# Kernel optimization log

Measured on AMD Instinct MI355X. Metric: run time of the kernel, lower is better.

## Reference

```python
import jax, jax.numpy as jnp
import numpy as np

NUM_HEADS = 16
EMBED_DIM = 1024
HEAD_DIM = EMBED_DIM // NUM_HEADS


def setup_inputs() -> dict:
    key = jax.random.key(0)
    ks = jax.random.split(key, 9)
    B, S, D = 2, 2048, EMBED_DIM
    s = 1.0 / np.sqrt(D)
    inp = {
        "x": jax.random.normal(ks[0], (B, S, D), dtype=jnp.float32),
        "Wq": jax.random.normal(ks[1], (D, D), dtype=jnp.float32) * s,
        "bq": jnp.zeros((D,), dtype=jnp.float32),
        "Wk": jax.random.normal(ks[2], (D, D), dtype=jnp.float32) * s,
        "bk": jnp.zeros((D,), dtype=jnp.float32),
        "Wv": jax.random.normal(ks[3], (D, D), dtype=jnp.float32) * s,
        "bv": jnp.zeros((D,), dtype=jnp.float32),
        "Wo": jax.random.normal(ks[4], (D, D), dtype=jnp.float32) * s,
        "bo": jnp.zeros((D,), dtype=jnp.float32),
    }
    return inp


def reference(x, Wq, bq, Wk, bk, Wv, bv, Wo, bo):
    B, S, D = x.shape
    H, Hd = NUM_HEADS, HEAD_DIM
    # projections (weights stored [in, out])
    q = (x @ Wq + bq).reshape(B, S, H, Hd).transpose(0, 2, 1, 3)  # [B,H,S,Hd]
    k = (x @ Wk + bk).reshape(B, S, H, Hd).transpose(0, 2, 1, 3)
    v = (x @ Wv + bv).reshape(B, S, H, Hd).transpose(0, 2, 1, 3)
    scores = jnp.einsum("bhqd,bhkd->bhqk", q, k) / jnp.sqrt(jnp.float32(Hd))
    causal = jnp.tril(jnp.ones((S, S), dtype=bool))  # True = keep
    scores = jnp.where(causal, scores, jnp.float32(-jnp.inf))
    attn = jax.nn.softmax(scores, axis=-1)
    ctx = jnp.einsum("bhqk,bhkd->bhqd", attn, v)  # [B,H,S,Hd]
    ctx = ctx.transpose(0, 2, 1, 3).reshape(B, S, D)
    return ctx @ Wo + bo
```

## Files before the change

### kernel.cpp

```cpp
#include <hip/hip_runtime.h>

#define NUMH 16
#define HD   64
#define SEQ  2048
#define NB   2
#define DIM  1024
#define MROWS (NB * SEQ)

typedef __attribute__((ext_vector_type(8))) short short8;
typedef __attribute__((ext_vector_type(4))) float f32x4;
typedef unsigned short u16;
typedef unsigned int u32;

__device__ inline u16 bf16_rn(float f) {
    unsigned u = __float_as_uint(f);
    return (u16)((u + 0x7FFFu + ((u >> 16) & 1u)) >> 16);
}
__device__ inline float bf16f(u16 h) {
    return __uint_as_float(((unsigned)h) << 16);
}

#define GLD16(gp, lp)                                                        \
    __builtin_amdgcn_global_load_lds(                                        \
        (const __attribute__((address_space(1))) void*)(gp),                 \
        (__attribute__((address_space(3))) void*)(lp), 16, 0, 0)

__global__ void convert_split(const float* __restrict__ in,
                              u16* __restrict__ hi, u16* __restrict__ lo, int n4)
{
    for (int i = blockIdx.x * blockDim.x + threadIdx.x; i < n4;
         i += gridDim.x * blockDim.x) {
        const float4 v = ((const float4*)in)[i];
        ushort4 h, l;
        h.x = bf16_rn(v.x); l.x = bf16_rn(v.x - bf16f(h.x));
        h.y = bf16_rn(v.y); l.y = bf16_rn(v.y - bf16f(h.y));
        h.z = bf16_rn(v.z); l.z = bf16_rn(v.z - bf16f(h.z));
        h.w = bf16_rn(v.w); l.w = bf16_rn(v.w - bf16f(h.w));
        ((ushort4*)hi)[i] = h;
        ((ushort4*)lo)[i] = l;
    }
}

__global__ __launch_bounds__(256)
void transpose_split(const float* __restrict__ W,
                     u16* __restrict__ th, u16* __restrict__ tl, float scale)
{
    __shared__ float Ls[32][33];
    const int tx = threadIdx.x & 31, ty = threadIdx.x >> 5;
    const int k0 = blockIdx.x * 32, n0 = blockIdx.y * 32;
#pragma unroll
    for (int i = 0; i < 4; ++i)
        Ls[ty + 8 * i][tx] = W[(size_t)(k0 + ty + 8 * i) * DIM + n0 + tx];
    __syncthreads();
#pragma unroll
    for (int i = 0; i < 4; ++i) {
        const float f = Ls[tx][ty + 8 * i] * scale;
        const u16 h = bf16_rn(f);
        const u16 l = bf16_rn(f - bf16f(h));
        th[(size_t)(n0 + ty + 8 * i) * DIM + k0 + tx] = h;
        tl[(size_t)(n0 + ty + 8 * i) * DIM + k0 + tx] = l;
    }
}

template<int EPI>
__global__ __launch_bounds__(256, 4)
void gemm_split(const u16* __restrict__ Ah, const u16* __restrict__ Al,
                const u16* __restrict__ Bh, const u16* __restrict__ Bl,
                const float* __restrict__ bias, float bscale,
                float* __restrict__ outF, u16* __restrict__ outH,
                u16* __restrict__ outL)
{
    __shared__ u16 AsH[128][32];
    __shared__ u16 AsL[128][32];
    __shared__ u16 BsH[64][32];
    __shared__ u16 BsL[64][32];

    const int tid  = threadIdx.x;
    const int m0   = blockIdx.x * 128;
    const int n0   = blockIdx.y * 64;
    const int wid  = tid >> 6;
    const int lane = tid & 63;
    const int wr   = wid >> 1;
    const int wc   = wid & 1;
    const int fr   = lane & 15;
    const int fg   = lane >> 4;
    const int K    = DIM;

    f32x4 acc[4][2];
#pragma unroll
    for (int i = 0; i < 4; ++i)
#pragma unroll
        for (int j = 0; j < 2; ++j) { f32x4 z = {0.f, 0.f, 0.f, 0.f}; acc[i][j] = z; }

    const int gr = (wid << 4) + (lane >> 2);
    const int gc = (lane & 3) * 8;

    for (int kt = 0; kt < K; kt += 32) {
        __syncthreads();
        GLD16(&Ah[(size_t)(m0 + gr) * K + kt + gc],      &AsH[(wid << 4)][0]);
        GLD16(&Ah[(size_t)(m0 + 64 + gr) * K + kt + gc], &AsH[64 + (wid << 4)][0]);
        GLD16(&Al[(size_t)(m0 + gr) * K + kt + gc],      &AsL[(wid << 4)][0]);
        GLD16(&Al[(size_t)(m0 + 64 + gr) * K + kt + gc], &AsL[64 + (wid << 4)][0]);
        GLD16(&Bh[(size_t)(n0 + gr) * K + kt + gc],      &BsH[(wid << 4)][0]);
        GLD16(&Bl[(size_t)(n0 + gr) * K + kt + gc],      &BsL[(wid << 4)][0]);
        __syncthreads();

        short8 afh[4], afl[4], bfh[2], bfl[2];
#pragma unroll
        for (int i = 0; i < 4; ++i) {
            afh[i] = *(const short8*)&AsH[wr * 64 + i * 16 + fr][fg * 8];
            afl[i] = *(const short8*)&AsL[wr * 64 + i * 16 + fr][fg * 8];
        }
#pragma unroll
        for (int j = 0; j < 2; ++j) {
            bfh[j] = *(const short8*)&BsH[wc * 32 + j * 16 + fr][fg * 8];
            bfl[j] = *(const short8*)&BsL[wc * 32 + j * 16 + fr][fg * 8];
        }
#pragma unroll
        for (int i = 0; i < 4; ++i)
#pragma unroll
            for (int j = 0; j < 2; ++j) {
                acc[i][j] = __builtin_amdgcn_mfma_f32_16x16x32_bf16(afl[i], bfh[j], acc[i][j], 0, 0, 0);
                acc[i][j] = __builtin_amdgcn_mfma_f32_16x16x32_bf16(afh[i], bfl[j], acc[i][j], 0, 0, 0);
                acc[i][j] = __builtin_amdgcn_mfma_f32_16x16x32_bf16(afh[i], bfh[j], acc[i][j], 0, 0, 0);
            }
    }

#pragma unroll
    for (int i = 0; i < 4; ++i)
#pragma unroll
        for (int j = 0; j < 2; ++j) {
            const int col = n0 + wc * 32 + j * 16 + fr;
            const float bv = bias[col] * bscale;
            if (EPI == 2) {
                const int row = m0 + wr * 64 + i * 16 + fg * 4;
                const int b  = row >> 11;
                const int s  = row & (SEQ - 1);
                const int hh = col >> 6;
                const int hd = col & (HD - 1);
                ushort4 pk;
                pk.x = bf16_rn(acc[i][j][0] + bv);
                pk.y = bf16_rn(acc[i][j][1] + bv);
                pk.z = bf16_rn(acc[i][j][2] + bv);
                pk.w = bf16_rn(acc[i][j][3] + bv);
                *(ushort4*)&outH[((size_t)(b * NUMH + hh) * HD + hd) * SEQ + s] = pk;
            } else {
#pragma unroll
                for (int r = 0; r < 4; ++r) {
                    const int row = m0 + wr * 64 + i * 16 + fg * 4 + r;
                    const float v = acc[i][j][r] + bv;
                    if (EPI == 0) {
                        outF[(size_t)row * DIM + col] = v;
                    } else {
                        const int b  = row >> 11;
                        const int s  = row & (SEQ - 1);
                        const int hh = col >> 6;
                        const int hd = col & (HD - 1);
                        const size_t idx = ((size_t)(b * NUMH + hh) * SEQ + s) * HD + hd;
                        const u16 hv = bf16_rn(v);
                        outH[idx] = hv;
                        outL[idx] = bf16_rn(v - bf16f(hv));
                    }
                }
            }
        }
}

__global__ __launch_bounds__(512, 4)
void attn_mfma4(const u16* __restrict__ Qh, const u16* __restrict__ Ql,
                const u16* __restrict__ Kh, const u16* __restrict__ Kl,
                const u16* __restrict__ Vt,
                u16* __restrict__ ctxH, u16* __restrict__ ctxL)
{
    __shared__ u16 KsH[64 * 64];
    __shared__ u16 KsL[64 * 64];
    __shared__ u16 Vs [64 * 64];

    const int tid  = threadIdx.x;
    const int w    = tid >> 6;
    const int lane = tid & 63;
    const int lc   = lane & 15;
    const int g    = lane >> 4;

    const int orig = blockIdx.x;
    const int swz  = (orig & 7) * 64 + (orig >> 3);
    const int bh   = swz >> 4;
    const int p    = swz & 15;
    const int qA   = p, qB = 31 - p;
    const int qt_w = (w < 4) ? qA : qB;
    const int wq   = w & 3;
    const int NT   = 32 - p;

    const int bb = bh >> 4, hq = bh & 15;
    const size_t kqBase = (size_t)bh * SEQ * HD;
    const size_t vBase  = (size_t)bh * HD * SEQ;

    short8 qh[2], ql[2];
    {
        const size_t ra = kqBase + (size_t)(qt_w * 64 + wq * 16 + lc) * HD;
        qh[0] = *(const short8*)&Qh[ra + g * 8];  qh[1] = *(const short8*)&Qh[ra + 32 + g * 8];
        ql[0] = *(const short8*)&Ql[ra + g * 8];  ql[1] = *(const short8*)&Ql[ra + 32 + g * 8];
    }

    f32x4 o[4];
#pragma unroll
    for (int f4 = 0; f4 < 4; ++f4) { f32x4 z = {0.f, 0.f, 0.f, 0.f}; o[f4] = z; }
    float mrun = -1e30f, lrun = 0.f;

    const int srow = tid >> 3;
    const int scol = (tid & 7) * 8;
    const int so   = srow * 64 + (scol ^ ((srow & 7) << 3));
    const int rsw  = (lc & 7) << 3;

    short8 pf0, pf1, pf2;
    auto LOADT = [&](int kt) {
        const size_t kg = kqBase + (size_t)(kt * 64 + srow) * HD + scol;
        pf0 = *(const short8*)&Kh[kg];
        pf1 = *(const short8*)&Kl[kg];
        const size_t vg = vBase + (size_t)srow * SEQ + kt * 64 + scol;
        pf2 = *(const short8*)&Vt[vg];
    };
    LOADT(0);

    const int a0 = (((g & 1) * 2 + 0) * 16 + lc) * 4;
    const int a1 = (((g & 1) * 2 + 1) * 16 + lc) * 4;
    const bool hi = ((g >> 1) & 1) != 0;

    for (int kt = 0; kt < NT; ++kt) {
        __syncthreads();
        *(short8*)&KsH[so] = pf0;
        *(short8*)&KsL[so] = pf1;
        *(short8*)&Vs [so] = pf2;
        __syncthreads();
        if (kt + 1 < NT) LOADT(kt + 1);

        if (kt <= qt_w) {
            const int k0 = kt * 64;

            f32x4 sf[4];
#pragma unroll
            for (int f4 = 0; f4 < 4; ++f4) {
                f32x4 a = {0.f, 0.f, 0.f, 0.f};
#pragma unroll
                for (int s2 = 0; s2 < 2; ++s2) {
                    const int off = (f4 * 16 + lc) * 64 + ((s2 * 32 + g * 8) ^ rsw);
                    const short8 kh = *(const short8*)&KsH[off];
                    const short8 kl = *(const short8*)&KsL[off];
                    a = __builtin_amdgcn_mfma_f32_16x16x32_bf16(kh, ql[s2], a, 0, 0, 0);
                    a = __builtin_amdgcn_mfma_f32_16x16x32_bf16(kl, qh[s2], a, 0, 0, 0);
                    a = __builtin_amdgcn_mfma_f32_16x16x32_bf16(kh, qh[s2], a, 0, 0, 0);
                }
                sf[f4] = a;
            }

            const bool diag = (kt == qt_w);
            const int  qg   = qt_w * 64 + wq * 16 + lc;
            float pm = -1e30f;
#pragma unroll
            for (int f4 = 0; f4 < 4; ++f4)
#pragma unroll
                for (int r = 0; r < 4; ++r) {
                    float sv = sf[f4][r];
                    if (diag && (k0 + f4 * 16 + g * 4 + r > qg)) sv = -1e30f;
                    sf[f4][r] = sv;
                    pm = fmaxf(pm, sv);
                }
            pm = fmaxf(pm, __shfl_xor(pm, 16));
            pm = fmaxf(pm, __shfl_xor(pm, 32));
            const float mn = fmaxf(mrun, pm);
            const float sc = __expf(mrun - mn);
            mrun = mn; lrun *= sc;
#pragma unroll
            for (int f4 = 0; f4 < 4; ++f4) o[f4] *= sc;

            float ps = 0.f;
            u32 pk[4][2];
#pragma unroll
            for (int f4 = 0; f4 < 4; ++f4)
#pragma unroll
                for (int pr = 0; pr < 2; ++pr) {
                    const float p0 = __expf(sf[f4][pr * 2 + 0] - mn);
                    const float p1 = __expf(sf[f4][pr * 2 + 1] - mn);
                    ps += p0 + p1;
                    pk[f4][pr] = (u32)bf16_rn(p0) | ((u32)bf16_rn(p1) << 16);
                }
            ps += __shfl_xor(ps, 16);
            ps += __shfl_xor(ps, 32);
            lrun += ps;

            u32 pb[2][4];
#pragma unroll
            for (int s2 = 0; s2 < 2; ++s2)
#pragma unroll
                for (int mm = 0; mm < 4; ++mm) {
                    const int addr = (mm < 2) ? a0 : a1;
                    const u32 t0 = (u32)__builtin_amdgcn_ds_bpermute(addr, (int)pk[s2 * 2 + 0][mm & 1]);
                    const u32 t1 = (u32)__builtin_amdgcn_ds_bpermute(addr, (int)pk[s2 * 2 + 1][mm & 1]);
                    pb[s2][mm] = hi ? t1 : t0;
                }

#pragma unroll
            for (int s2 = 0; s2 < 2; ++s2) {
                union { u32 u[4]; short8 s; } ua;
#pragma unroll
                for (int mm = 0; mm < 4; ++mm) ua.u[mm] = pb[s2][mm];
#pragma unroll
                for (int f4 = 0; f4 < 4; ++f4) {
                    const int off = (f4 * 16 + lc) * 64 + ((s2 * 32 + g * 8) ^ rsw);
                    const short8 vv = *(const short8*)&Vs[off];
                    o[f4] = __builtin_amdgcn_mfma_f32_16x16x32_bf16(vv, ua.s, o[f4], 0, 0, 0);
                }
            }
        }
    }

    const float iv = 1.f / lrun;
    const size_t rowA = (size_t)bb * SEQ + qt_w * 64 + wq * 16 + lc;
#pragma unroll
    for (int f4 = 0; f4 < 4; ++f4) {
        const int colb = hq * HD + f4 * 16 + g * 4;
        ushort4 h4, l4;
#pragma unroll
        for (int r = 0; r < 4; ++r) {
            const float v = o[f4][r] * iv;
            const u16 hv = bf16_rn(v);
            ((u16*)&h4)[r] = hv;
            ((u16*)&l4)[r] = bf16_rn(v - bf16f(hv));
        }
        *(ushort4*)&ctxH[rowA * DIM + colb] = h4;
        *(ushort4*)&ctxL[rowA * DIM + colb] = l4;
    }
}

extern "C" void kernel_launch(void* const* d_in, const int* in_sizes, int n_in,
                              void* d_out, int out_size, void* d_ws, size_t ws_size,
                              hipStream_t stream)
{
    const float* x  = (const float*)d_in[0];
    const float* Wq = (const float*)d_in[1];
    const float* bq = (const float*)d_in[2];
    const float* Wk = (const float*)d_in[3];
    const float* bk = (const float*)d_in[4];
    const float* Wv = (const float*)d_in[5];
    const float* bv = (const float*)d_in[6];
    const float* Wo = (const float*)d_in[7];
    const float* bo = (const float*)d_in[8];

    char* base = (char*)d_ws;
    const size_t MB = 1024 * 1024;
    u16* Qh_ = (u16*)(base + 0 * MB);
    u16* Ql_ = (u16*)(base + 8 * MB);
    u16* Kh_ = (u16*)(base + 16 * MB);
    u16* Kl_ = (u16*)(base + 24 * MB);
    u16* Vt_ = (u16*)(base + 32 * MB);
    u16* xh  = (u16*)(base + 40 * MB);
    u16* xl  = (u16*)(base + 48 * MB);
    u16* Wth = (u16*)(base + 56 * MB);
    u16* Wtl = (u16*)(base + 58 * MB);

    dim3 blk(256);
    dim3 gg(MROWS / 128, DIM / 64);
    dim3 gt(DIM / 32, DIM / 32);

    hipLaunchKernelGGL(convert_split, dim3(2048), blk, 0, stream,
                       x, xh, xl, MROWS * DIM / 4);

    hipLaunchKernelGGL(transpose_split, gt, blk, 0, stream, Wq, Wth, Wtl, 0.125f);
    hipLaunchKernelGGL((gemm_split<1>), gg, blk, 0, stream,
                       xh, xl, Wth, Wtl, bq, 0.125f, nullptr, Qh_, Ql_);

    hipLaunchKernelGGL(transpose_split, gt, blk, 0, stream, Wk, Wth, Wtl, 1.0f);
    hipLaunchKernelGGL((gemm_split<1>), gg, blk, 0, stream,
                       xh, xl, Wth, Wtl, bk, 1.0f, nullptr, Kh_, Kl_);

    hipLaunchKernelGGL(transpose_split, gt, blk, 0, stream, Wv, Wth, Wtl, 1.0f);
    hipLaunchKernelGGL((gemm_split<2>), gg, blk, 0, stream,
                       xh, xl, Wth, Wtl, bv, 1.0f, nullptr, Vt_, nullptr);

    hipLaunchKernelGGL(attn_mfma4, dim3(NB * NUMH * 16), dim3(512), 0, stream,
                       Qh_, Ql_, Kh_, Kl_, Vt_, xh, xl);

    hipLaunchKernelGGL(transpose_split, gt, blk, 0, stream, Wo, Wth, Wtl, 1.0f);
    hipLaunchKernelGGL((gemm_split<0>), gg, blk, 0, stream,
                       xh, xl, Wth, Wtl, bo, 1.0f, (float*)d_out, nullptr, nullptr);
}
```

Measured before the change: 319.7 us.

## Double-buffer LDS in GEMM and attention, reassign causal tiles, use exp2 softmax

Both the split-bf16 GEMM and the attention kernel now use two LDS buffers per operand. The next tile is staged while the current one is consumed, which removes one barrier per iteration and hides global-load latency. The attention kernel changes its work mapping: each block now handles two adjacent query tiles, with the heaviest launched first, in place of the paired p/31-p balancing. The softmax folds log2(e) into the Q scale so it can use exp2f. The cost is doubled LDS per block and a lower GEMM occupancy hint (3 instead of 4), and the new tile mapping may balance load across blocks less evenly.

Result: slower. 335.6 us (+5.0%).

```diff
diff --git a/kernel.cpp b/kernel.cpp
--- a/kernel.cpp
+++ b/kernel.cpp
@@ -6,6 +6,7 @@
 #define NB   2
 #define DIM  1024
 #define MROWS (NB * SEQ)
+#define QSCALE 0.180336880111f
 
 typedef __attribute__((ext_vector_type(8))) short short8;
 typedef __attribute__((ext_vector_type(4))) float f32x4;
@@ -63,17 +64,17 @@
 }
 
 template<int EPI>
-__global__ __launch_bounds__(256, 4)
+__global__ __launch_bounds__(256, 3)
 void gemm_split(const u16* __restrict__ Ah, const u16* __restrict__ Al,
                 const u16* __restrict__ Bh, const u16* __restrict__ Bl,
                 const float* __restrict__ bias, float bscale,
                 float* __restrict__ outF, u16* __restrict__ outH,
                 u16* __restrict__ outL)
 {
-    __shared__ u16 AsH[128][32];
-    __shared__ u16 AsL[128][32];
-    __shared__ u16 BsH[64][32];
-    __shared__ u16 BsL[64][32];
+    __shared__ u16 AsH[2][128][32];
+    __shared__ u16 AsL[2][128][32];
+    __shared__ u16 BsH[2][64][32];
+    __shared__ u16 BsL[2][64][32];
 
     const int tid  = threadIdx.x;
     const int m0   = blockIdx.x * 128;
@@ -95,26 +96,32 @@
     const int gr = (wid << 4) + (lane >> 2);
     const int gc = (lane & 3) * 8;
 
+    auto STAGE = [&](int buf, int kt) {
+        GLD16(&Ah[(size_t)(m0 + gr) * K + kt + gc],      &AsH[buf][(wid << 4)][0]);
+        GLD16(&Ah[(size_t)(m0 + 64 + gr) * K + kt + gc], &AsH[buf][64 + (wid << 4)][0]);
+        GLD16(&Al[(size_t)(m0 + gr) * K + kt + gc],      &AsL[buf][(wid << 4)][0]);
+        GLD16(&Al[(size_t)(m0 + 64 + gr) * K + kt + gc], &AsL[buf][64 + (wid << 4)][0]);
+        GLD16(&Bh[(size_t)(n0 + gr) * K + kt + gc],      &BsH[buf][(wid << 4)][0]);
+        GLD16(&Bl[(size_t)(n0 + gr) * K + kt + gc],      &BsL[buf][(wid << 4)][0]);
+    };
+
+    STAGE(0, 0);
+    __syncthreads();
+
     for (int kt = 0; kt < K; kt += 32) {
-        __syncthreads();
-        GLD16(&Ah[(size_t)(m0 + gr) * K + kt + gc],      &AsH[(wid << 4)][0]);
-        GLD16(&Ah[(size_t)(m0 + 64 + gr) * K + kt + gc], &AsH[64 + (wid << 4)][0]);
-        GLD16(&Al[(size_t)(m0 + gr) * K + kt + gc],      &AsL[(wid << 4)][0]);
-        GLD16(&Al[(size_t)(m0 + 64 + gr) * K + kt + gc], &AsL[64 + (wid << 4)][0]);
-        GLD16(&Bh[(size_t)(n0 + gr) * K + kt + gc],      &BsH[(wid << 4)][0]);
-        GLD16(&Bl[(size_t)(n0 + gr) * K + kt + gc],      &BsL[(wid << 4)][0]);
-        __syncthreads();
+        const int cur = (kt >> 5) & 1;
+        if (kt + 32 < K) STAGE(cur ^ 1, kt + 32);
 
         short8 afh[4], afl[4], bfh[2], bfl[2];
 #pragma unroll
         for (int i = 0; i < 4; ++i) {
-            afh[i] = *(const short8*)&AsH[wr * 64 + i * 16 + fr][fg * 8];
-            afl[i] = *(const short8*)&AsL[wr * 64 + i * 16 + fr][fg * 8];
+            afh[i] = *(const short8*)&AsH[cur][wr * 64 + i * 16 + fr][fg * 8];
+            afl[i] = *(const short8*)&AsL[cur][wr * 64 + i * 16 + fr][fg * 8];
         }
 #pragma unroll
         for (int j = 0; j < 2; ++j) {
-            bfh[j] = *(const short8*)&BsH[wc * 32 + j * 16 + fr][fg * 8];
-            bfl[j] = *(const short8*)&BsL[wc * 32 + j * 16 + fr][fg * 8];
+            bfh[j] = *(const short8*)&BsH[cur][wc * 32 + j * 16 + fr][fg * 8];
+            bfl[j] = *(const short8*)&BsL[cur][wc * 32 + j * 16 + fr][fg * 8];
         }
 #pragma unroll
         for (int i = 0; i < 4; ++i)
@@ -124,6 +131,8 @@
                 acc[i][j] = __builtin_amdgcn_mfma_f32_16x16x32_bf16(afh[i], bfl[j], acc[i][j], 0, 0, 0);
                 acc[i][j] = __builtin_amdgcn_mfma_f32_16x16x32_bf16(afh[i], bfh[j], acc[i][j], 0, 0, 0);
             }
+
+        __syncthreads();
     }
 
 #pragma unroll
@@ -167,14 +176,14 @@
 }
 
 __global__ __launch_bounds__(512, 4)
-void attn_mfma4(const u16* __restrict__ Qh, const u16* __restrict__ Ql,
+void attn_mfma5(const u16* __restrict__ Qh, const u16* __restrict__ Ql,
                 const u16* __restrict__ Kh, const u16* __restrict__ Kl,
                 const u16* __restrict__ Vt,
                 u16* __restrict__ ctxH, u16* __restrict__ ctxL)
 {
-    __shared__ u16 KsH[64 * 64];
-    __shared__ u16 KsL[64 * 64];
-    __shared__ u16 Vs [64 * 64];
+    __shared__ u16 KsH[2][64 * 64];
+    __shared__ u16 KsL[2][64 * 64];
+    __shared__ u16 Vs [2][64 * 64];
 
     const int tid  = threadIdx.x;
     const int w    = tid >> 6;
@@ -183,13 +192,12 @@
     const int g    = lane >> 4;
 
     const int orig = blockIdx.x;
-    const int swz  = (orig & 7) * 64 + (orig >> 3);
-    const int bh   = swz >> 4;
-    const int p    = swz & 15;
-    const int qA   = p, qB = 31 - p;
-    const int qt_w = (w < 4) ? qA : qB;
+    const int j    = orig >> 3;
+    const int bh   = (orig & 7) * 4 + (j >> 4);
+    const int p    = 15 - (j & 15);
+    const int qt_w = 2 * p + (w >> 2);
     const int wq   = w & 3;
-    const int NT   = 32 - p;
+    const int NT   = 2 * p + 2;
 
     const int bb = bh >> 4, hq = bh & 15;
     const size_t kqBase = (size_t)bh * SEQ * HD;
@@ -220,18 +228,19 @@
         const size_t vg = vBase + (size_t)srow * SEQ + kt * 64 + scol;
         pf2 = *(const short8*)&Vt[vg];
     };
-    LOADT(0);
 
     const int a0 = (((g & 1) * 2 + 0) * 16 + lc) * 4;
     const int a1 = (((g & 1) * 2 + 1) * 16 + lc) * 4;
     const bool hi = ((g >> 1) & 1) != 0;
 
+    LOADT(0);
+    *(short8*)&KsH[0][so] = pf0;
+    *(short8*)&KsL[0][so] = pf1;
+    *(short8*)&Vs [0][so] = pf2;
+    __syncthreads();
+
     for (int kt = 0; kt < NT; ++kt) {
-        __syncthreads();
-        *(short8*)&KsH[so] = pf0;
-        *(short8*)&KsL[so] = pf1;
-        *(short8*)&Vs [so] = pf2;
-        __syncthreads();
+        const int cur = kt & 1;
         if (kt + 1 < NT) LOADT(kt + 1);
 
         if (kt <= qt_w) {
@@ -244,8 +253,8 @@
 #pragma unroll
                 for (int s2 = 0; s2 < 2; ++s2) {
                     const int off = (f4 * 16 + lc) * 64 + ((s2 * 32 + g * 8) ^ rsw);
-                    const short8 kh = *(const short8*)&KsH[off];
-                    const short8 kl = *(const short8*)&KsL[off];
+                    const short8 kh = *(const short8*)&KsH[cur][off];
+                    const short8 kl = *(const short8*)&KsL[cur][off];
                     a = __builtin_amdgcn_mfma_f32_16x16x32_bf16(kh, ql[s2], a, 0, 0, 0);
                     a = __builtin_amdgcn_mfma_f32_16x16x32_bf16(kl, qh[s2], a, 0, 0, 0);
                     a = __builtin_amdgcn_mfma_f32_16x16x32_bf16(kh, qh[s2], a, 0, 0, 0);
@@ -268,7 +277,7 @@
             pm = fmaxf(pm, __shfl_xor(pm, 16));
             pm = fmaxf(pm, __shfl_xor(pm, 32));
             const float mn = fmaxf(mrun, pm);
-            const float sc = __expf(mrun - mn);
+            const float sc = exp2f(mrun - mn);
             mrun = mn; lrun *= sc;
 #pragma unroll
             for (int f4 = 0; f4 < 4; ++f4) o[f4] *= sc;
@@ -279,8 +288,8 @@
             for (int f4 = 0; f4 < 4; ++f4)
 #pragma unroll
                 for (int pr = 0; pr < 2; ++pr) {
-                    const float p0 = __expf(sf[f4][pr * 2 + 0] - mn);
-                    const float p1 = __expf(sf[f4][pr * 2 + 1] - mn);
+                    const float p0 = exp2f(sf[f4][pr * 2 + 0] - mn);
+                    const float p1 = exp2f(sf[f4][pr * 2 + 1] - mn);
                     ps += p0 + p1;
                     pk[f4][pr] = (u32)bf16_rn(p0) | ((u32)bf16_rn(p1) << 16);
                 }
@@ -307,11 +316,18 @@
 #pragma unroll
                 for (int f4 = 0; f4 < 4; ++f4) {
                     const int off = (f4 * 16 + lc) * 64 + ((s2 * 32 + g * 8) ^ rsw);
-                    const short8 vv = *(const short8*)&Vs[off];
+                    const short8 vv = *(const short8*)&Vs[cur][off];
                     o[f4] = __builtin_amdgcn_mfma_f32_16x16x32_bf16(vv, ua.s, o[f4], 0, 0, 0);
                 }
             }
         }
+
+        if (kt + 1 < NT) {
+            *(short8*)&KsH[cur ^ 1][so] = pf0;
+            *(short8*)&KsL[cur ^ 1][so] = pf1;
+            *(short8*)&Vs [cur ^ 1][so] = pf2;
+        }
+        __syncthreads();
     }
 
     const float iv = 1.f / lrun;
@@ -365,9 +381,9 @@
     hipLaunchKernelGGL(convert_split, dim3(2048), blk, 0, stream,
                        x, xh, xl, MROWS * DIM / 4);
 
-    hipLaunchKernelGGL(transpose_split, gt, blk, 0, stream, Wq, Wth, Wtl, 0.125f);
+    hipLaunchKernelGGL(transpose_split, gt, blk, 0, stream, Wq, Wth, Wtl, QSCALE);
     hipLaunchKernelGGL((gemm_split<1>), gg, blk, 0, stream,
-                       xh, xl, Wth, Wtl, bq, 0.125f, nullptr, Qh_, Ql_);
+                       xh, xl, Wth, Wtl, bq, QSCALE, nullptr, Qh_, Ql_);
 
     hipLaunchKernelGGL(transpose_split, gt, blk, 0, stream, Wk, Wth, Wtl, 1.0f);
     hipLaunchKernelGGL((gemm_split<1>), gg, blk, 0, stream,
@@ -377,7 +393,7 @@
     hipLaunchKernelGGL((gemm_split<2>), gg, blk, 0, stream,
                        xh, xl, Wth, Wtl, bv, 1.0f, nullptr, Vt_, nullptr);
 
-    hipLaunchKernelGGL(attn_mfma4, dim3(NB * NUMH * 16), dim3(512), 0, stream,
+    hipLaunchKernelGGL(attn_mfma5, dim3(NB * NUMH * 16), dim3(512), 0, stream,
                        Qh_, Ql_, Kh_, Kl_, Vt_, xh, xl);
 
     hipLaunchKernelGGL(transpose_split, gt, blk, 0, stream, Wo, Wth, Wtl, 1.0f);
```
